# Performance work log

Measured on AMD Instinct MI355X. Metric: run time of the kernel, lower is better.

The kernel has to match this reference:

```python
import jax, jax.numpy as jnp
import numpy as np


def setup_inputs() -> dict:
    key = jax.random.key(0)
    ks = jax.random.split(key, 6)
    B, T, C, NL = 2, 2048, 2048, 512
    s = 0.02
    return {
        "x": jax.random.normal(ks[0], (B, T, C), jnp.float32),
        "W_dq": jax.random.normal(ks[1], (NL, C), jnp.float32) * s,
        "W_dkv": jax.random.normal(ks[2], (NL, C), jnp.float32) * s,
        "W_uk": jax.random.normal(ks[3], (C, NL), jnp.float32) * s,
        "W_uv": jax.random.normal(ks[4], (C, NL), jnp.float32) * s,
        "W_o": jax.random.normal(ks[5], (C, C), jnp.float32) * s,
        "n_head": 16,
    }


def reference(x, W_dq, W_dkv, W_uk, W_uv, W_o, n_head):
    B, T, C = x.shape
    nl = W_dkv.shape[0]
    nh = n_head
    hs = C // nh
    # Absorbed key projection: (W_dq^T @ W_uk^T @ W_uk) -> [C, nl] -> [nh, hs, nl]
    k_abs = (W_dq.T @ W_uk.T @ W_uk).reshape(nh, hs, nl)
    # Absorbed value/output projection: (W_uv^T @ W_o^T) -> [nl, C] -> [nh, nl, hs]
    v_abs = jnp.transpose((W_uv.T @ W_o.T).reshape(nl, nh, hs), (1, 0, 2))
    # Latent KV cache: [B, T, nl]
    c_kv = x @ W_dkv.T
    # Queries: raw x split into heads (matches reference: no W_dq/W_uq applied to q)
    q = x.reshape(B, T, nh, hs).transpose(0, 2, 1, 3)  # [B, nh, T, hs]
    # Scores via chained low-rank matmuls: q @ k_abs @ c_kv^T
    scores = jnp.einsum('bhtd,hdl,bsl->bhts', q, k_abs, c_kv) / jnp.sqrt(
        jnp.asarray(hs, x.dtype))
    # Causal mask + softmax (dropout p=0 -> identity)
    mask = jnp.tril(jnp.ones((T, T), dtype=bool))
    scores = jnp.where(mask, scores, -jnp.inf)
    attn = jax.nn.softmax(scores, axis=-1)  # [B, nh, T, T]
    # Output: attn @ c_kv @ v_abs
    y = jnp.einsum('bhts,bsl,hld->bhtd', attn, c_kv, v_abs)  # [B, nh, T, hs]
    y = y.transpose(0, 2, 1, 3).reshape(B, T, C)
    return (y, c_kv)
```

## Files before the change

### kernel.cpp

```cpp
#include <hip/hip_runtime.h>
#include <stdint.h>

typedef __attribute__((ext_vector_type(8))) short short8;
typedef __attribute__((ext_vector_type(4))) short short4v;
typedef __attribute__((ext_vector_type(2))) short short2v;
typedef __attribute__((ext_vector_type(4))) float f32x4;
typedef __attribute__((ext_vector_type(8))) __bf16 bf16x8;

__device__ __forceinline__ short f2bf(float f) {
  unsigned u = __builtin_bit_cast(unsigned, f);
  u = (u + 0x7FFFu + ((u >> 16) & 1u)) >> 16;
  return (short)u;
}

__device__ __forceinline__ short f2bf_fast(float f) {
  return (short)((__builtin_bit_cast(unsigned, f) + 0x8000u) >> 16);
}

__device__ __forceinline__ f32x4 mfma16(short8 a, short8 b, f32x4 c) {
  return __builtin_amdgcn_mfma_f32_16x16x32_bf16(
      __builtin_bit_cast(bf16x8, a), __builtin_bit_cast(bf16x8, b), c, 0, 0, 0);
}

__device__ __forceinline__ void gload_lds16(const void* g, void* l) {
  __builtin_amdgcn_global_load_lds(
      (const __attribute__((address_space(1))) unsigned int*)g,
      (__attribute__((address_space(3))) unsigned int*)l, 16, 0, 0);
}

__global__ __launch_bounds__(256) void conv3(
    const float* __restrict__ x, const float* __restrict__ wdkv,
    const float* __restrict__ wo,
    short* __restrict__ xb, short* __restrict__ wdkvb, short* __restrict__ wob) {
  int i = blockIdx.x * 256 + threadIdx.x;
  const float* in; short* out; int off;
  if (i < 2097152)      { in = x;    out = xb;    off = i; }
  else if (i < 2359296) { in = wdkv; out = wdkvb; off = i - 2097152; }
  else                  { in = wo;   out = wob;   off = i - 2359296; }
  f32x4 v = ((const f32x4*)in)[off];
  short4v o;
  o[0] = f2bf(v[0]); o[1] = f2bf(v[1]); o[2] = f2bf(v[2]); o[3] = f2bf(v[3]);
  ((short4v*)out)[off] = o;
}

__global__ __launch_bounds__(256) void trans_w3(
    const float* __restrict__ Wuk, const float* __restrict__ Wdq,
    const float* __restrict__ Wuv,
    short* __restrict__ wukT, short* __restrict__ wdqT, short* __restrict__ wuvT)
{
  const int z = blockIdx.y;
  const float* in; short* out; int R, C;
  if (z == 0)      { in = Wuk; out = wukT; R = 2048; C = 512; }
  else if (z == 1) { in = Wdq; out = wdqT; R = 512;  C = 2048; }
  else             { in = Wuv; out = wuvT; R = 2048; C = 512; }
  const int tpc = C >> 6;
  const int r0 = (blockIdx.x / tpc) << 6, c0 = (blockIdx.x % tpc) << 6;
  __shared__ float tile[64][65];
  const int tid = threadIdx.x;
#pragma unroll
  for (int i = 0; i < 4; ++i) {
    int idx = tid + i * 256;
    int row = idx >> 4, col4 = (idx & 15) * 4;
    f32x4 v = *(const f32x4*)(in + (size_t)(r0 + row) * C + c0 + col4);
    tile[row][col4] = v[0]; tile[row][col4 + 1] = v[1];
    tile[row][col4 + 2] = v[2]; tile[row][col4 + 3] = v[3];
  }
  __syncthreads();
#pragma unroll
  for (int i = 0; i < 4; ++i) {
    int idx = tid + i * 256;
    int crow = idx >> 4, r4 = (idx & 15) * 4;
    short4v o;
    o[0] = f2bf(tile[r4][crow]);     o[1] = f2bf(tile[r4 + 1][crow]);
    o[2] = f2bf(tile[r4 + 2][crow]); o[3] = f2bf(tile[r4 + 3][crow]);
    *(short4v*)(out + (size_t)(c0 + crow) * R + r0 + r4) = o;
  }
}

__global__ __launch_bounds__(256) void trans_vabs(const short* __restrict__ in,
                                                  short* __restrict__ out) {
  const int c0 = blockIdx.x << 6, l0 = blockIdx.y << 6;
  __shared__ short tile[64][66];
  const int tid = threadIdx.x;
#pragma unroll
  for (int i = 0; i < 8; ++i) {
    int idx = tid + i * 256;
    int row = idx >> 5, col2 = (idx & 31) * 2;
    short2v v = *(const short2v*)(in + (size_t)(l0 + row) * 2048 + c0 + col2);
    tile[row][col2] = v[0]; tile[row][col2 + 1] = v[1];
  }
  __syncthreads();
  const int h = c0 >> 7, d0 = c0 & 127;
  short* ob = out + ((size_t)h << 16) + (size_t)d0 * 512 + l0;
#pragma unroll
  for (int i = 0; i < 8; ++i) {
    int idx = tid + i * 256;
    int crow = idx >> 5, l2 = (idx & 31) * 2;
    short2v v;
    v[0] = tile[l2][crow]; v[1] = tile[l2 + 1][crow];
    *(short2v*)(ob + (size_t)crow * 512 + l2) = v;
  }
}


__device__ __forceinline__ void gemm128_body(
    const short* A, const short* B, float* Cf, short* Cb,
    int K, int lda, int ldb, int ldc, int bx, int by, float scale)
{
  const int tid = threadIdx.x, wid = tid >> 6, L = tid & 63;
  const int g = L >> 4, r16 = L & 15, wr = wid >> 1, wc = wid & 1;
  const int rl = L >> 3, ru = L & 7;

  __shared__ short Asm[128 * 64], Bsm[128 * 64];
  char* Ab = (char*)Asm;
  char* Bb = (char*)Bsm;

  const f32x4 fz = {0.f, 0.f, 0.f, 0.f};
  f32x4 acc[4][4];
#pragma unroll
  for (int m = 0; m < 4; ++m)
#pragma unroll
    for (int n = 0; n < 4; ++n) acc[m][n] = fz;

  const int aRow0 = bx * 128, bRow0 = by * 128;

  for (int kt = 0; kt < K; kt += 64) {
#pragma unroll
    for (int i = 0; i < 4; ++i) {
      int row = i * 32 + wid * 8 + rl;
      gload_lds16(A + (size_t)(aRow0 + row) * lda + kt + ((ru ^ rl) * 8),
                  Ab + (i * 32 + wid * 8) * 128);
    }
#pragma unroll
    for (int i = 0; i < 4; ++i) {
      int row = i * 32 + wid * 8 + rl;
      gload_lds16(B + (size_t)(bRow0 + row) * ldb + kt + ((ru ^ rl) * 8),
                  Bb + (i * 32 + wid * 8) * 128);
    }
    __syncthreads();
#pragma unroll
    for (int kk = 0; kk < 2; ++kk) {
      short8 a[4], b2[4];
#pragma unroll
      for (int m = 0; m < 4; ++m) {
        int row = wr * 64 + m * 16 + r16;
        a[m] = *(const short8*)(Ab + row * 128 + (((kk * 4 + g) ^ (row & 7)) << 4));
      }
#pragma unroll
      for (int n = 0; n < 4; ++n) {
        int row = wc * 64 + n * 16 + r16;
        b2[n] = *(const short8*)(Bb + row * 128 + (((kk * 4 + g) ^ (row & 7)) << 4));
      }
#pragma unroll
      for (int m = 0; m < 4; ++m)
#pragma unroll
        for (int n = 0; n < 4; ++n) acc[m][n] = mfma16(a[m], b2[n], acc[m][n]);
    }
    __syncthreads();
  }

#pragma unroll
  for (int m = 0; m < 4; ++m) {
    int row0 = aRow0 + wr * 64 + m * 16 + g * 4;
#pragma unroll
    for (int n = 0; n < 4; ++n) {
      int col = bRow0 + wc * 64 + n * 16 + r16;
#pragma unroll
      for (int e = 0; e < 4; ++e) {
        long idx = (long)(row0 + e) * ldc + col;
        float v = acc[m][n][e] * scale;
        if (Cf) Cf[idx] = v;
        if (Cb) Cb[idx] = f2bf(v);
      }
    }
  }
}

__device__ __forceinline__ void gemm64_body(
    const short* A, const short* B, float* Cf, short* Cb,
    int K, int lda, int ldb, int ldc, int bx, int by, float scale)
{
  const int tid = threadIdx.x, wid = tid >> 6, L = tid & 63;
  const int g = L >> 4, r16 = L & 15, wr = wid >> 1, wc = wid & 1;

  __shared__ short Asm[64 * 64], Bsm[64 * 64];
  char* Ab = (char*)Asm;
  char* Bb = (char*)Bsm;

  const f32x4 fz = {0.f, 0.f, 0.f, 0.f};
  f32x4 acc[2][2] = {{fz, fz}, {fz, fz}};
  const int aRow0 = bx * 64, bRow0 = by * 64;

  for (int kt = 0; kt < K; kt += 64) {
#pragma unroll
    for (int i = 0; i < 2; ++i) {
      int ug = i * 256 + wid * 64;
      int row = (ug + L) >> 3, u = (ug + L) & 7;
      gload_lds16(A + (size_t)(aRow0 + row) * lda + kt + ((u ^ (row & 7)) * 8),
                  Ab + ug * 16);
    }
#pragma unroll
    for (int i = 0; i < 2; ++i) {
      int ug = i * 256 + wid * 64;
      int row = (ug + L) >> 3, u = (ug + L) & 7;
      gload_lds16(B + (size_t)(bRow0 + row) * ldb + kt + ((u ^ (row & 7)) * 8),
                  Bb + ug * 16);
    }
    __syncthreads();
#pragma unroll
    for (int kk = 0; kk < 2; ++kk) {
      short8 a[2], b2[2];
#pragma unroll
      for (int m = 0; m < 2; ++m) {
        int row = wr * 32 + m * 16 + r16;
        a[m] = *(const short8*)(Ab + row * 128 + (((kk * 4 + g) ^ (row & 7)) << 4));
      }
#pragma unroll
      for (int n = 0; n < 2; ++n) {
        int row = wc * 32 + n * 16 + r16;
        b2[n] = *(const short8*)(Bb + row * 128 + (((kk * 4 + g) ^ (row & 7)) << 4));
      }
#pragma unroll
      for (int m = 0; m < 2; ++m)
#pragma unroll
        for (int n = 0; n < 2; ++n) acc[m][n] = mfma16(a[m], b2[n], acc[m][n]);
    }
    __syncthreads();
  }

#pragma unroll
  for (int m = 0; m < 2; ++m) {
    int row0 = aRow0 + wr * 32 + m * 16 + g * 4;
#pragma unroll
    for (int n = 0; n < 2; ++n) {
      int col = bRow0 + wc * 32 + n * 16 + r16;
#pragma unroll
      for (int e = 0; e < 4; ++e) {
        long idx = (long)(row0 + e) * ldc + col;
        float v = acc[m][n][e] * scale;
        if (Cf) Cf[idx] = v;
        if (Cb) Cb[idx] = f2bf(v);
      }
    }
  }
}

__global__ __launch_bounds__(256) void gemm_jobs3(
    const short* __restrict__ wukT, const short* __restrict__ wuvT,
    const short* __restrict__ wo, const short* __restrict__ x_bf,
    const short* __restrict__ wdkv,
    short* __restrict__ m1, short* __restrict__ vflat,
    float* __restrict__ ckv_f, short* __restrict__ ckvb)
{
  const int bid = blockIdx.x;
  const short *A, *B; short* Cb; float* Cf; int bx, by, ldc;
  if (bid < 64)       { A = wukT; B = wukT; Cb = m1;    Cf = nullptr;
                        bx = bid >> 3;         by = bid & 7;         ldc = 512; }
  else if (bid < 320) { A = wuvT; B = wo;   Cb = vflat; Cf = nullptr;
                        bx = (bid - 64) >> 5;  by = (bid - 64) & 31; ldc = 2048; }
  else                { A = x_bf; B = wdkv; Cb = ckvb;  Cf = ckv_f;
                        bx = (bid - 320) >> 3; by = (bid - 320) & 7; ldc = 512; }
  gemm64_body(A, B, Cf, Cb, 2048, 2048, 2048, ldc, bx, by, 1.0f);
}

__global__ __launch_bounds__(256) void gemm_kabs(
    const short* __restrict__ wdqT, const short* __restrict__ m1,
    short* __restrict__ kabs)
{
  gemm64_body(wdqT, m1, nullptr, kabs, 512, 512, 512, 512,
              blockIdx.x, blockIdx.y, 0.08838834764831845f * 1.4426950408889634f);
}

__global__ __launch_bounds__(256) void gemm_keffveff(
    const short* __restrict__ ckvb, const short* __restrict__ kabs,
    const short* __restrict__ vabsT,
    short* __restrict__ keffT, short* __restrict__ veffT)
{
  const int bz = blockIdx.z;
  const short *A, *B; short* C; int ldc, bx, by;
  if (bz < 32) {
    int b = bz >> 4, h = bz & 15;
    A = ckvb + (size_t)b * 2048 * 512;
    B = kabs + (size_t)h * 128 * 512;
    C = keffT + (size_t)bz * 2048 * 128;
    ldc = 128; bx = blockIdx.x; by = 0;
  } else {
    int bh = bz - 32, b = bh >> 4, h = bh & 15;
    A = vabsT + (size_t)h * 128 * 512;
    B = ckvb + (size_t)b * 2048 * 512;
    C = veffT + (size_t)bh * 128 * 2048;
    ldc = 2048; bx = 0; by = blockIdx.x;
  }
  gemm128_body(A, B, nullptr, C, 512, 512, 512, ldc, bx, by, 1.0f);
}

__global__ __launch_bounds__(256) void flash_d128(
    const short* __restrict__ x_bf,
    const short* __restrict__ kT,
    const short* __restrict__ vT,
    float* __restrict__ y)
{
  const int f = blockIdx.x;
  const int qt = (f < 256) ? (f >> 5) : 15 - ((f - 256) >> 5);
  const int bh = f & 31, b = bh >> 4, h = bh & 15;
  const int tid = threadIdx.x, wid = tid >> 6, L = tid & 63, g = L >> 4, r16 = L & 15;
  const int qw = qt * 128 + wid * 32;

  __shared__ char lds[81920];

  const char* kp0;
  const char* vp0;
  {
    const char* kbase = (const char*)(kT + (size_t)bh * (2048 * 128));
    const char* vbase = (const char*)(vT + (size_t)bh * (128 * 2048));
    kp0 = kbase + (wid * 4 + g) * 256 + ((r16 ^ (wid * 4 + g)) << 4);
    vp0 = vbase + (size_t)(wid * 8 + (L >> 3)) * 4096 + (((L & 7) ^ (L >> 3)) << 4);
  }

  auto stage = [&](int c) {
    const int base = 16384 + c * 32768 + wid * 1024;
#pragma unroll
    for (int i = 0; i < 4; ++i)
      gload_lds16(kp0 + i * 4096, lds + base + i * 4096);
#pragma unroll
    for (int i = 0; i < 4; ++i)
      gload_lds16(vp0 + (size_t)i * 131072, lds + base + 16384 + i * 4096);
    kp0 += 16384;
    vp0 += 128;
  };

  int kfo[4], vfo[2], pao[2][2], pwo[2][4];
#pragma unroll
  for (int ks = 0; ks < 4; ++ks)
    kfo[ks] = 16384 + r16 * 256 + (((ks * 4 + g) ^ r16) << 4);
#pragma unroll
  for (int kk = 0; kk < 2; ++kk)
    vfo[kk] = 32768 + r16 * 128 + (((kk * 4 + g) ^ (r16 & 7)) << 4);
#pragma unroll
  for (int m = 0; m < 2; ++m)
#pragma unroll
    for (int kk = 0; kk < 2; ++kk)
      pao[m][kk] = wid * 4096 + m * 2048 + r16 * 128 + (((kk * 4 + g) ^ (r16 & 7)) << 4);
#pragma unroll
  for (int m = 0; m < 2; ++m)
#pragma unroll
    for (int e = 0; e < 4; ++e) {
      int qrow = m * 16 + g * 4 + e;
      pwo[m][e] = wid * 4096 + qrow * 128 + ((r16 * 2) ^ ((qrow & 7) << 4));
    }

  short8 qf[2][4];
#pragma unroll
  for (int m = 0; m < 2; ++m)
#pragma unroll
    for (int ks = 0; ks < 4; ++ks)
      qf[m][ks] = *(const short8*)(x_bf +
          (size_t)(b * 2048 + qw + m * 16 + r16) * 2048 + h * 128 + ks * 32 + g * 8);

  const f32x4 fz = {0.f, 0.f, 0.f, 0.f};
  f32x4 acc[2][8];
#pragma unroll
  for (int m = 0; m < 2; ++m)
#pragma unroll
    for (int n = 0; n < 8; ++n) acc[m][n] = fz;
  f32x4 acc_l[2] = {fz, fz};

  short8 ones;
#pragma unroll
  for (int i = 0; i < 8; ++i) ones[i] = (short)0x3F80;

  const int nkt = 2 * qt + 2;
  stage(0);

  for (int kt = 0; kt < nkt; ++kt) {
    const int c = kt & 1, co = c * 32768, s0 = kt * 64;

    if (kt + 1 < nkt) {
      stage(c ^ 1);
      asm volatile("s_waitcnt vmcnt(8)" ::: "memory");
    } else {
      asm volatile("s_waitcnt vmcnt(0)" ::: "memory");
    }
    __builtin_amdgcn_s_barrier();

    f32x4 s[2][4] = {{fz, fz, fz, fz}, {fz, fz, fz, fz}};
    __builtin_amdgcn_s_setprio(1);
#pragma unroll
    for (int ks = 0; ks < 4; ++ks) {
      const char* kb = lds + co + kfo[ks];
#pragma unroll
      for (int n = 0; n < 4; ++n) {
        short8 kf = *(const short8*)(kb + n * 4096);
        s[0][n] = mfma16(qf[0][ks], kf, s[0][n]);
        s[1][n] = mfma16(qf[1][ks], kf, s[1][n]);
      }
    }
    __builtin_amdgcn_s_setprio(0);

    if (s0 + 63 > qw) {
#pragma unroll
      for (int m = 0; m < 2; ++m)
#pragma unroll
        for (int n = 0; n < 4; ++n)
#pragma unroll
          for (int e = 0; e < 4; ++e)
            if (s0 + n * 16 + r16 > qw + m * 16 + g * 4 + e) s[m][n][e] = -3e38f;
    }

#pragma unroll
    for (int m = 0; m < 2; ++m)
#pragma unroll
      for (int n = 0; n < 4; ++n)
#pragma unroll
        for (int e = 0; e < 4; ++e) {
          float p = exp2f(s[m][n][e]);
          *(short*)(lds + (pwo[m][e] ^ (n << 5))) = f2bf_fast(p);
        }
    short8 pa[2][2];
#pragma unroll
    for (int m = 0; m < 2; ++m)
#pragma unroll
      for (int kk = 0; kk < 2; ++kk)
        pa[m][kk] = *(const short8*)(lds + pao[m][kk]);

    __builtin_amdgcn_s_setprio(1);
#pragma unroll
    for (int m = 0; m < 2; ++m)
#pragma unroll
      for (int kk = 0; kk < 2; ++kk) acc_l[m] = mfma16(pa[m][kk], ones, acc_l[m]);
#pragma unroll
    for (int kk = 0; kk < 2; ++kk) {
      const char* vb = lds + co + vfo[kk];
#pragma unroll
      for (int n = 0; n < 8; ++n) {
        short8 vf = *(const short8*)(vb + n * 2048);
        acc[0][n] = mfma16(pa[0][kk], vf, acc[0][n]);
        acc[1][n] = mfma16(pa[1][kk], vf, acc[1][n]);
      }
    }
    __builtin_amdgcn_s_setprio(0);

    asm volatile("s_waitcnt lgkmcnt(0)" ::: "memory");
    __builtin_amdgcn_s_barrier();
  }

  float inv[2][4];
#pragma unroll
  for (int m = 0; m < 2; ++m)
#pragma unroll
    for (int e = 0; e < 4; ++e) inv[m][e] = 1.f / acc_l[m][e];
#pragma unroll
  for (int m = 0; m < 2; ++m)
#pragma unroll
    for (int n = 0; n < 8; ++n)
#pragma unroll
      for (int e = 0; e < 4; ++e) {
        int row = qw + m * 16 + g * 4 + e;
        y[(size_t)(b * 2048 + row) * 2048 + h * 128 + n * 16 + r16] =
            acc[m][n][e] * inv[m][e];
      }
}


extern "C" void kernel_launch(void* const* d_in, const int* in_sizes, int n_in,
                              void* d_out, int out_size, void* d_ws, size_t ws_size,
                              hipStream_t stream) {
  const float* x    = (const float*)d_in[0];
  const float* Wdq  = (const float*)d_in[1];
  const float* Wdkv = (const float*)d_in[2];
  const float* Wuk  = (const float*)d_in[3];
  const float* Wuv  = (const float*)d_in[4];
  const float* Wo   = (const float*)d_in[5];
  float* y     = (float*)d_out;
  float* ckv_f = y + (size_t)2 * 2048 * 2048;

  char* w = (char*)d_ws;
  auto alloc = [&](size_t bytes) { char* p = w; w += (bytes + 255) & ~(size_t)255; return p; };
  short* x_bf   = (short*)alloc((size_t)2 * 2048 * 2048 * 2);
  short* wdkv   = (short*)alloc((size_t)512 * 2048 * 2);
  short* wukT   = (short*)alloc((size_t)512 * 2048 * 2);
  short* wdqT   = (short*)alloc((size_t)2048 * 512 * 2);
  short* wuvT   = (short*)alloc((size_t)512 * 2048 * 2);
  short* wo     = (short*)alloc((size_t)2048 * 2048 * 2);
  short* m1     = (short*)alloc((size_t)512 * 512 * 2);
  short* kabs   = (short*)alloc((size_t)2048 * 512 * 2);
  short* vflat  = (short*)alloc((size_t)512 * 2048 * 2);
  short* vabsT  = (short*)alloc((size_t)16 * 128 * 512 * 2);
  short* ckvb   = (short*)alloc((size_t)2 * 2048 * 512 * 2);
  short* keffT  = (short*)alloc((size_t)32 * 2048 * 128 * 2);
  short* veffT  = (short*)alloc((size_t)32 * 128 * 2048 * 2);

  conv3<<<13312, 256, 0, stream>>>(x, Wdkv, Wo, x_bf, wdkv, wo);
  trans_w3<<<dim3(256, 3), 256, 0, stream>>>(Wuk, Wdq, Wuv, wukT, wdqT, wuvT);

  gemm_jobs3<<<832, 256, 0, stream>>>(wukT, wuvT, wo, x_bf, wdkv,
                                      m1, vflat, ckv_f, ckvb);
  gemm_kabs<<<dim3(32, 8), 256, 0, stream>>>(wdqT, m1, kabs);
  trans_vabs<<<dim3(32, 8), 256, 0, stream>>>(vflat, vabsT);

  gemm_keffveff<<<dim3(16, 1, 64), 256, 0, stream>>>(ckvb, kabs, vabsT, keffT, veffT);

  flash_d128<<<512, 256, 0, stream>>>(x_bf, keffT, veffT, y);
}
```

Baseline: 163.1 us.

## Rebalance flash attention with paired causal tiles and use 128-tile GEMMs

The flash kernel now gives each block two query segments, tile pp and tile 15-pp, so every block does the same amount of causal work. Each block covers 64 query rows (16 per wave) instead of 128, with the r bit picking the half, which halves per-wave registers and LDS. The combined projection GEMM switches from 64x64 to 128x128 tiles, cutting its grid from 832 to 208 blocks. The cost is that K/V tiles are reloaded for each segment and the GEMM launches fewer blocks than the GPU has CUs.

```diff
diff --git a/kernel.cpp b/kernel.cpp
--- a/kernel.cpp
+++ b/kernel.cpp
@@ -254,13 +254,13 @@
 {
   const int bid = blockIdx.x;
   const short *A, *B; short* Cb; float* Cf; int bx, by, ldc;
-  if (bid < 64)       { A = wukT; B = wukT; Cb = m1;    Cf = nullptr;
-                        bx = bid >> 3;         by = bid & 7;         ldc = 512; }
-  else if (bid < 320) { A = wuvT; B = wo;   Cb = vflat; Cf = nullptr;
-                        bx = (bid - 64) >> 5;  by = (bid - 64) & 31; ldc = 2048; }
-  else                { A = x_bf; B = wdkv; Cb = ckvb;  Cf = ckv_f;
-                        bx = (bid - 320) >> 3; by = (bid - 320) & 7; ldc = 512; }
-  gemm64_body(A, B, Cf, Cb, 2048, 2048, 2048, ldc, bx, by, 1.0f);
+  if (bid < 16)      { A = wukT; B = wukT; Cb = m1;    Cf = nullptr;
+                       bx = bid >> 2;        by = bid & 3;         ldc = 512; }
+  else if (bid < 80) { A = wuvT; B = wo;   Cb = vflat; Cf = nullptr;
+                       bx = (bid - 16) >> 4; by = (bid - 16) & 15; ldc = 2048; }
+  else               { A = x_bf; B = wdkv; Cb = ckvb;  Cf = ckv_f;
+                       bx = (bid - 80) >> 2; by = (bid - 80) & 3;  ldc = 512; }
+  gemm128_body(A, B, Cf, Cb, 2048, 2048, 2048, ldc, bx, by, 1.0f);
 }
 
 __global__ __launch_bounds__(256) void gemm_kabs(
@@ -301,164 +301,141 @@
     float* __restrict__ y)
 {
   const int f = blockIdx.x;
-  const int qt = (f < 256) ? (f >> 5) : 15 - ((f - 256) >> 5);
-  const int bh = f & 31, b = bh >> 4, h = bh & 15;
+  const int r = f & 1, bh = (f >> 1) & 31, pp = f >> 6;
+  const int b = bh >> 4, h = bh & 15;
   const int tid = threadIdx.x, wid = tid >> 6, L = tid & 63, g = L >> 4, r16 = L & 15;
-  const int qw = qt * 128 + wid * 32;
-
-  __shared__ char lds[81920];
-
-  const char* kp0;
-  const char* vp0;
-  {
-    const char* kbase = (const char*)(kT + (size_t)bh * (2048 * 128));
-    const char* vbase = (const char*)(vT + (size_t)bh * (128 * 2048));
-    kp0 = kbase + (wid * 4 + g) * 256 + ((r16 ^ (wid * 4 + g)) << 4);
-    vp0 = vbase + (size_t)(wid * 8 + (L >> 3)) * 4096 + (((L & 7) ^ (L >> 3)) << 4);
-  }
-
-  auto stage = [&](int c) {
-    const int base = 16384 + c * 32768 + wid * 1024;
-#pragma unroll
-    for (int i = 0; i < 4; ++i)
-      gload_lds16(kp0 + i * 4096, lds + base + i * 4096);
-#pragma unroll
-    for (int i = 0; i < 4; ++i)
-      gload_lds16(vp0 + (size_t)i * 131072, lds + base + 16384 + i * 4096);
-    kp0 += 16384;
-    vp0 += 128;
-  };
-
-  int kfo[4], vfo[2], pao[2][2], pwo[2][4];
+
+  __shared__ char lds[73728];
+
+  const char* kbase = (const char*)(kT + (size_t)bh * (2048 * 128));
+  const char* vbase = (const char*)(vT + (size_t)bh * (128 * 2048));
+
+  int kfo[4], vfo[2], pao[2], pwo[4];
 #pragma unroll
   for (int ks = 0; ks < 4; ++ks)
-    kfo[ks] = 16384 + r16 * 256 + (((ks * 4 + g) ^ r16) << 4);
-#pragma unroll
-  for (int kk = 0; kk < 2; ++kk)
-    vfo[kk] = 32768 + r16 * 128 + (((kk * 4 + g) ^ (r16 & 7)) << 4);
-#pragma unroll
-  for (int m = 0; m < 2; ++m)
-#pragma unroll
-    for (int kk = 0; kk < 2; ++kk)
-      pao[m][kk] = wid * 4096 + m * 2048 + r16 * 128 + (((kk * 4 + g) ^ (r16 & 7)) << 4);
-#pragma unroll
-  for (int m = 0; m < 2; ++m)
-#pragma unroll
-    for (int e = 0; e < 4; ++e) {
-      int qrow = m * 16 + g * 4 + e;
-      pwo[m][e] = wid * 4096 + qrow * 128 + ((r16 * 2) ^ ((qrow & 7) << 4));
-    }
-
-  short8 qf[2][4];
-#pragma unroll
-  for (int m = 0; m < 2; ++m)
+    kfo[ks] = 8192 + r16 * 256 + (((ks * 4 + g) ^ r16) << 4);
+#pragma unroll
+  for (int kk = 0; kk < 2; ++kk) {
+    vfo[kk] = 24576 + r16 * 128 + (((kk * 4 + g) ^ (r16 & 7)) << 4);
+    pao[kk] = wid * 2048 + r16 * 128 + (((kk * 4 + g) ^ (r16 & 7)) << 4);
+  }
+#pragma unroll
+  for (int e = 0; e < 4; ++e) {
+    int qrow = g * 4 + e;
+    pwo[e] = wid * 2048 + qrow * 128 + ((r16 * 2) ^ ((qrow & 7) << 4));
+  }
+
+  const int kLaneOff = (wid * 4 + g) * 256 + ((r16 ^ (wid * 4 + g)) << 4);
+  const size_t vLaneOff = (size_t)(wid * 8 + (L >> 3)) * 4096 + (((L & 7) ^ (L >> 3)) << 4);
+
+  short8 ones;
+#pragma unroll
+  for (int i = 0; i < 8; ++i) ones[i] = (short)0x3F80;
+  const f32x4 fz = {0.f, 0.f, 0.f, 0.f};
+
+  for (int seg = 0; seg < 2; ++seg) {
+    const int qt = seg ? 15 - pp : pp;
+    const int qw = qt * 128 + r * 64 + wid * 16;
+    const int nkt = 2 * qt + 1 + r;
+
+    short8 qf[4];
 #pragma unroll
     for (int ks = 0; ks < 4; ++ks)
-      qf[m][ks] = *(const short8*)(x_bf +
-          (size_t)(b * 2048 + qw + m * 16 + r16) * 2048 + h * 128 + ks * 32 + g * 8);
-
-  const f32x4 fz = {0.f, 0.f, 0.f, 0.f};
-  f32x4 acc[2][8];
-#pragma unroll
-  for (int m = 0; m < 2; ++m)
-#pragma unroll
-    for (int n = 0; n < 8; ++n) acc[m][n] = fz;
-  f32x4 acc_l[2] = {fz, fz};
-
-  short8 ones;
-#pragma unroll
-  for (int i = 0; i < 8; ++i) ones[i] = (short)0x3F80;
-
-  const int nkt = 2 * qt + 2;
-  stage(0);
-
-  for (int kt = 0; kt < nkt; ++kt) {
-    const int c = kt & 1, co = c * 32768, s0 = kt * 64;
-
-    if (kt + 1 < nkt) {
-      stage(c ^ 1);
-      asm volatile("s_waitcnt vmcnt(8)" ::: "memory");
-    } else {
-      asm volatile("s_waitcnt vmcnt(0)" ::: "memory");
-    }
-    __builtin_amdgcn_s_barrier();
-
-    f32x4 s[2][4] = {{fz, fz, fz, fz}, {fz, fz, fz, fz}};
-    __builtin_amdgcn_s_setprio(1);
-#pragma unroll
-    for (int ks = 0; ks < 4; ++ks) {
-      const char* kb = lds + co + kfo[ks];
-#pragma unroll
-      for (int n = 0; n < 4; ++n) {
-        short8 kf = *(const short8*)(kb + n * 4096);
-        s[0][n] = mfma16(qf[0][ks], kf, s[0][n]);
-        s[1][n] = mfma16(qf[1][ks], kf, s[1][n]);
-      }
-    }
-    __builtin_amdgcn_s_setprio(0);
-
-    if (s0 + 63 > qw) {
-#pragma unroll
-      for (int m = 0; m < 2; ++m)
+      qf[ks] = *(const short8*)(x_bf +
+          (size_t)(b * 2048 + qw + r16) * 2048 + h * 128 + ks * 32 + g * 8);
+
+    f32x4 acc[8];
+#pragma unroll
+    for (int n = 0; n < 8; ++n) acc[n] = fz;
+    f32x4 acc_l = fz;
+
+    const char* kp = kbase + kLaneOff;
+    const char* vp = vbase + vLaneOff;
+
+    auto stage = [&](int c) {
+      const int base = 8192 + c * 32768 + wid * 1024;
+#pragma unroll
+      for (int i = 0; i < 4; ++i)
+        gload_lds16(kp + i * 4096, lds + base + i * 4096);
+#pragma unroll
+      for (int i = 0; i < 4; ++i)
+        gload_lds16(vp + (size_t)i * 131072, lds + base + 16384 + i * 4096);
+      kp += 16384;
+      vp += 128;
+    };
+
+    stage(0);
+
+    for (int kt = 0; kt < nkt; ++kt) {
+      const int c = kt & 1, co = c * 32768, s0 = kt * 64;
+
+      if (kt + 1 < nkt) {
+        stage(c ^ 1);
+        asm volatile("s_waitcnt vmcnt(8)" ::: "memory");
+      } else {
+        asm volatile("s_waitcnt vmcnt(0)" ::: "memory");
+      }
+      __builtin_amdgcn_s_barrier();
+
+      f32x4 s[4] = {fz, fz, fz, fz};
+      __builtin_amdgcn_s_setprio(1);
+#pragma unroll
+      for (int ks = 0; ks < 4; ++ks) {
+        const char* kb = lds + co + kfo[ks];
 #pragma unroll
         for (int n = 0; n < 4; ++n)
+          s[n] = mfma16(qf[ks], *(const short8*)(kb + n * 4096), s[n]);
+      }
+      __builtin_amdgcn_s_setprio(0);
+
+      if (s0 + 63 > qw) {
+#pragma unroll
+        for (int n = 0; n < 4; ++n)
 #pragma unroll
           for (int e = 0; e < 4; ++e)
-            if (s0 + n * 16 + r16 > qw + m * 16 + g * 4 + e) s[m][n][e] = -3e38f;
-    }
-
-#pragma unroll
-    for (int m = 0; m < 2; ++m)
+            if (s0 + n * 16 + r16 > qw + g * 4 + e) s[n][e] = -3e38f;
+      }
+
 #pragma unroll
       for (int n = 0; n < 4; ++n)
 #pragma unroll
         for (int e = 0; e < 4; ++e) {
-          float p = exp2f(s[m][n][e]);
-          *(short*)(lds + (pwo[m][e] ^ (n << 5))) = f2bf_fast(p);
+          float p = exp2f(s[n][e]);
+          *(short*)(lds + (pwo[e] ^ (n << 5))) = f2bf_fast(p);
         }
-    short8 pa[2][2];
-#pragma unroll
-    for (int m = 0; m < 2; ++m)
+      short8 pa[2];
 #pragma unroll
       for (int kk = 0; kk < 2; ++kk)
-        pa[m][kk] = *(const short8*)(lds + pao[m][kk]);
-
-    __builtin_amdgcn_s_setprio(1);
-#pragma unroll
-    for (int m = 0; m < 2; ++m)
-#pragma unroll
-      for (int kk = 0; kk < 2; ++kk) acc_l[m] = mfma16(pa[m][kk], ones, acc_l[m]);
-#pragma unroll
-    for (int kk = 0; kk < 2; ++kk) {
-      const char* vb = lds + co + vfo[kk];
-#pragma unroll
-      for (int n = 0; n < 8; ++n) {
-        short8 vf = *(const short8*)(vb + n * 2048);
-        acc[0][n] = mfma16(pa[0][kk], vf, acc[0][n]);
-        acc[1][n] = mfma16(pa[1][kk], vf, acc[1][n]);
-      }
-    }
-    __builtin_amdgcn_s_setprio(0);
-
-    asm volatile("s_waitcnt lgkmcnt(0)" ::: "memory");
-    __builtin_amdgcn_s_barrier();
-  }
-
-  float inv[2][4];
-#pragma unroll
-  for (int m = 0; m < 2; ++m)
-#pragma unroll
-    for (int e = 0; e < 4; ++e) inv[m][e] = 1.f / acc_l[m][e];
-#pragma unroll
-  for (int m = 0; m < 2; ++m)
+        pa[kk] = *(const short8*)(lds + pao[kk]);
+
+      __builtin_amdgcn_s_setprio(1);
+#pragma unroll
+      for (int kk = 0; kk < 2; ++kk) acc_l = mfma16(pa[kk], ones, acc_l);
+#pragma unroll
+      for (int kk = 0; kk < 2; ++kk) {
+        const char* vb = lds + co + vfo[kk];
+#pragma unroll
+        for (int n = 0; n < 8; ++n)
+          acc[n] = mfma16(pa[kk], *(const short8*)(vb + n * 2048), acc[n]);
+      }
+      __builtin_amdgcn_s_setprio(0);
+
+      asm volatile("s_waitcnt lgkmcnt(0)" ::: "memory");
+      __builtin_amdgcn_s_barrier();
+    }
+
+    float inv[4];
+#pragma unroll
+    for (int e = 0; e < 4; ++e) inv[e] = 1.f / acc_l[e];
 #pragma unroll
     for (int n = 0; n < 8; ++n)
 #pragma unroll
       for (int e = 0; e < 4; ++e) {
-        int row = qw + m * 16 + g * 4 + e;
+        int row = qw + g * 4 + e;
         y[(size_t)(b * 2048 + row) * 2048 + h * 128 + n * 16 + r16] =
-            acc[m][n][e] * inv[m][e];
-      }
+            acc[n][e] * inv[e];
+      }
+  }
 }
 
 
@@ -493,7 +470,7 @@
   conv3<<<13312, 256, 0, stream>>>(x, Wdkv, Wo, x_bf, wdkv, wo);
   trans_w3<<<dim3(256, 3), 256, 0, stream>>>(Wuk, Wdq, Wuv, wukT, wdqT, wuvT);
 
-  gemm_jobs3<<<832, 256, 0, stream>>>(wukT, wuvT, wo, x_bf, wdkv,
+  gemm_jobs3<<<208, 256, 0, stream>>>(wukT, wuvT, wo, x_bf, wdkv,
                                       m1, vflat, ckv_f, ckvb);
   gemm_kabs<<<dim3(32, 8), 256, 0, stream>>>(wdqT, m1, kabs);
   trans_vabs<<<dim3(32, 8), 256, 0, stream>>>(vflat, vabsT);
```

Result: slower. 169.0 us (+3.6%).
